# Optimization experiments

Measured on AMD Instinct MI355X. Metric: run time of the kernel, lower is better.

## Reference

```python
import jax, jax.numpy as jnp
import numpy as np
from jax import lax

H = 40            # hidden_size
IN = 257          # input_size / output bins
GRID_SIZE = 5     # efficient-kan defaults
SPLINE_ORDER = 3


def make_grid(in_features):
    # efficient-kan grid: arange(-k, G+k+1) * h + grid_range[0], grid_range=[-1,1]
    h = 2.0 / GRID_SIZE
    g = jnp.arange(-SPLINE_ORDER, GRID_SIZE + SPLINE_ORDER + 1, dtype=jnp.float32) * h - 1.0
    return jnp.broadcast_to(g, (in_features, g.shape[0]))  # (in, G+2k+1)


def b_splines(x, grid):
    # x: (N, in); grid: (in, G+2k+1) -> bases: (N, in, G+k) via Cox-de Boor
    xe = x[..., None]
    bases = ((xe >= grid[:, :-1]) & (xe < grid[:, 1:])).astype(x.dtype)
    for k in range(1, SPLINE_ORDER + 1):
        left = (xe - grid[:, :-(k + 1)]) / (grid[:, k:-1] - grid[:, :-(k + 1)])
        right = (grid[:, k + 1:] - xe) / (grid[:, k + 1:] - grid[:, 1:-k])
        bases = left * bases[..., :-1] + right * bases[..., 1:]
    return bases


def kan_linear(x, base_w, spline_w, scaler):
    # base_w: (out, in); spline_w: (out, in, G+k); scaler: (out, in)
    shp = x.shape
    x2 = x.reshape(-1, shp[-1])
    grid = make_grid(shp[-1])
    base = jax.nn.silu(x2) @ base_w.T
    sp = b_splines(x2, grid)                      # (N, in, G+k)
    scaled = spline_w * scaler[..., None]         # (out, in, G+k)
    spline = jnp.einsum('nig,oig->no', sp, scaled)
    out = base + spline
    return out.reshape(*shp[:-1], base_w.shape[0])


def gru_cell(x, h, Wih, Whh, bih, bhh):
    # torch GRUCell: gates ordered r, z, n
    gi = x @ Wih.T + bih
    gh = h @ Whh.T + bhh
    ir, iz, in_ = jnp.split(gi, 3, axis=-1)
    hr, hz, hn = jnp.split(gh, 3, axis=-1)
    r = jax.nn.sigmoid(ir + hr)
    z = jax.nn.sigmoid(iz + hz)
    n = jnp.tanh(in_ + r * hn)
    return (1.0 - z) * n + z * h


def run_gru(x_tbf, p0, p1):
    # x_tbf: (T, B, F); 2-layer stacked GRU scan, returns top-layer states (T, B, H)
    B = x_tbf.shape[1]
    def step(carry, xt):
        h0, h1 = carry
        h0 = gru_cell(xt, h0, *p0)
        h1 = gru_cell(h0, h1, *p1)
        return (h0, h1), h1
    init = (jnp.zeros((B, H), x_tbf.dtype), jnp.zeros((B, H), x_tbf.dtype))
    _, hs = lax.scan(step, init, x_tbf)
    return hs


def setup_inputs() -> dict:
    key = jax.random.key(0)
    ks = jax.random.split(key, 32)
    B, T = 64, 600
    s = 1.0 / np.sqrt(H)
    u = lambda k, shp: jax.random.uniform(k, shp, jnp.float32, -s, s)
    inp = {}
    inp['x'] = jax.random.normal(ks[0], (B, T, IN), jnp.float32)
    inp['lengths'] = jax.random.randint(ks[1], (B,), 1, T + 1, jnp.int32)
    i = 2
    for pre, insz in [('f0', IN), ('f1', H), ('b0', IN), ('b1', H)]:
        inp[pre + '_Wih'] = u(ks[i], (3 * H, insz)); i += 1
        inp[pre + '_Whh'] = u(ks[i], (3 * H, H)); i += 1
        inp[pre + '_bih'] = u(ks[i], (3 * H,)); i += 1
        inp[pre + '_bhh'] = u(ks[i], (3 * H,)); i += 1
    G = GRID_SIZE + SPLINE_ORDER
    inp['kan1_base'] = jax.random.normal(ks[i], (2 * H, 2 * H)) * 0.1; i += 1
    inp['kan1_spline'] = jax.random.normal(ks[i], (2 * H, 2 * H, G)) * 0.1; i += 1
    inp['kan1_scaler'] = jnp.ones((2 * H, 2 * H), jnp.float32)
    inp['kan2_base'] = jax.random.normal(ks[i], (IN, 2 * H)) * 0.1; i += 1
    inp['kan2_spline'] = jax.random.normal(ks[i], (IN, 2 * H, G)) * 0.1; i += 1
    inp['kan2_scaler'] = jnp.ones((IN, 2 * H), jnp.float32)
    inp['slope'] = jnp.ones((IN,), jnp.float32)
    return inp


def reference(x, lengths,
              f0_Wih, f0_Whh, f0_bih, f0_bhh,
              f1_Wih, f1_Whh, f1_bih, f1_bhh,
              b0_Wih, b0_Whh, b0_bih, b0_bhh,
              b1_Wih, b1_Whh, b1_bih, b1_bhh,
              kan1_base, kan1_spline, kan1_scaler,
              kan2_base, kan2_spline, kan2_scaler,
              slope):
    # lengths is unused by the original forward (kept for signature parity)
    xt = jnp.transpose(x, (1, 0, 2))  # (T, B, IN)
    hf = run_gru(xt, (f0_Wih, f0_Whh, f0_bih, f0_bhh), (f1_Wih, f1_Whh, f1_bih, f1_bhh))
    hb = run_gru(xt[::-1], (b0_Wih, b0_Whh, b0_bih, b0_bhh), (b1_Wih, b1_Whh, b1_bih, b1_bhh))
    # original stores concat(ht_f(i), ht_b(i)) at out[:, i]; ht_b(i) is step i of the
    # reversed-input scan, so NO flip of hb here.
    out = jnp.concatenate([hf, hb], axis=-1)        # (T, B, 2H)
    out = jnp.transpose(out, (1, 0, 2))             # (B, T, 2H)
    out = kan_linear(out, kan1_base, kan1_spline, kan1_scaler)
    out = kan_linear(out, kan2_base, kan2_spline, kan2_scaler)
    return 1.2 * jax.nn.sigmoid(slope * out)
```

## Files before the change

### kernel.cpp

```cpp
#include <hip/hip_runtime.h>
#include <cstdint>
#include <cstddef>

typedef unsigned short u16;
typedef unsigned int u32;
typedef __attribute__((ext_vector_type(8))) short short8;
typedef __attribute__((ext_vector_type(4))) float floatx4;
typedef __attribute__((ext_vector_type(2))) float float2v;

#define NROWS 38400

#define OFF_FLAG 0u
#define OFF_GI   64u
#define OFF_HCAT 36864064u
#define OFF_B1A  49152064u
#define OFF_B1B  49446976u
#define OFF_B2   49741888u
#define OFF_B3   49977408u

template<int N> struct IC { static constexpr int v = N; };

__device__ inline float bf2f(u16 u){ union{u32 i; float f;} v; v.i = ((u32)u)<<16; return v.f; }
__device__ inline u16 f2bf(float f){
  u32 u = __float_as_uint(f);
  return (u16)((u + 0x7FFFu + ((u>>16)&1u)) >> 16);
}
__device__ inline float lodf(const void* p, size_t i, int isbf){
  return isbf ? bf2f(((const u16*)p)[i]) : ((const float*)p)[i];
}
__device__ inline float rcpf(float x){ return __builtin_amdgcn_rcpf(x); }
__device__ inline float sigm(float x){ return rcpf(1.0f+__expf(-x)); }
__device__ inline float tanh_(float x){
  float e = __expf(-2.0f*fabsf(x)); float t = (1.0f-e)*rcpf(1.0f+e); return x<0.f ? -t : t;
}

__global__ void detect_kernel(const u16* __restrict__ xx, int* __restrict__ flag){
  const int l = threadIdx.x;
  const u16 w = xx[2*l];
  const int e = (w>>7)&0xFF;
  const unsigned long long m = __ballot(e >= 100 && e <= 133);
  if (l == 0) *flag = (__popcll(m) >= 32) ? 1 : 0;
}

__global__ void prep_kernel(const void* __restrict__ f0Wih, const void* __restrict__ b0Wih,
                            const void* __restrict__ k1b, const void* __restrict__ k1s, const void* __restrict__ k1sc,
                            const void* __restrict__ k2b, const void* __restrict__ k2s, const void* __restrict__ k2sc,
                            const int* __restrict__ flag,
                            u16* __restrict__ B1a, u16* __restrict__ B1b,
                            u16* __restrict__ B2, u16* __restrict__ B3)
{
  const int isbf = *flag;
  const int idx = blockIdx.x*256 + threadIdx.x;
  if (idx < 73728){
    const int j = idx/288, k = idx - j*288;
    float w = 0.f;
    if (k < 257 && j < 240)
      w = (j < 120) ? lodf(f0Wih, (size_t)j*257+k, isbf) : lodf(b0Wih, (size_t)(j-120)*257+k, isbf);
    const u16 hi = f2bf(w); const u16 lo = f2bf(w - bf2f(hi));
    B1a[(size_t)j*576 + 2*k] = hi; B1a[(size_t)j*576 + 2*k+1] = hi;
    B1b[(size_t)j*576 + 2*k] = lo; B1b[(size_t)j*576 + 2*k+1] = 0;
  } else if (idx < 132608){
    const int t = idx - 73728; const int n = t/736, m = t - n*736;
    float v = 0.f;
    if (m < 80) v = lodf(k1b, (size_t)n*80+m, isbf);
    else if (m >= 96){ const int m2 = m-96, i = m2>>3, g = m2&7;
      v = lodf(k1s, ((size_t)n*80+i)*8+g, isbf) * lodf(k1sc, (size_t)n*80+i, isbf); }
    const u16 vv = f2bf(v);
    B2[(size_t)n*1472 + 2*m] = vv; B2[(size_t)n*1472 + 2*m+1] = vv;
  } else {
    const int t = idx - 132608; const int n = t/736, m = t - n*736;
    float v = 0.f;
    if (n < 257){
      if (m < 80) v = lodf(k2b, (size_t)n*80+m, isbf);
      else if (m >= 96){ const int m2 = m-96, i = m2>>3, g = m2&7;
        v = lodf(k2s, ((size_t)n*80+i)*8+g, isbf) * lodf(k2sc, (size_t)n*80+i, isbf); }
    }
    const u16 vv = f2bf(v);
    B3[(size_t)n*1472 + 2*m] = vv; B3[(size_t)n*1472 + 2*m+1] = vv;
  }
}

__launch_bounds__(256)
__global__ void g1_kernel(const void* __restrict__ x, const u16* __restrict__ B1a, const u16* __restrict__ B1b,
                          const void* __restrict__ f0bih, const void* __restrict__ b0bih,
                          const int* __restrict__ flag, float* __restrict__ gi)
{
  __shared__ __attribute__((aligned(16))) u16 As[32][584];
  const int isbf = *flag;
  const int tid = threadIdx.x;
  const size_t r0 = (size_t)blockIdx.x * 32;
  const int w = tid>>6, l = tid&63, m16 = l&15, q4 = l>>4;
  const int cnt = (w<3)?4:3;
  const int ntlo = w*4;

  short8 bz;
  #pragma unroll
  for (int q=0;q<8;++q) bz[q]=0;
  short8 baC[4], bbC[4], baN[4], bbN[4];
  #pragma unroll
  for (int j=0;j<4;++j){ baC[j]=bz; bbC[j]=bz; baN[j]=bz; bbN[j]=bz; }
  #pragma unroll
  for (int j=0;j<4;++j) if (j<cnt){
    baC[j] = *(const short8*)&B1a[(size_t)((ntlo+j)*16+m16)*576 + q4*8];
    if (!isbf) bbC[j] = *(const short8*)&B1b[(size_t)((ntlo+j)*16+m16)*576 + q4*8];
  }

  {
    const int row = tid>>3, kk = tid&7;
    #pragma unroll
    for (int it=0; it<36; ++it){
      const int k = kk + it*8;
      const float v = (k < 257) ? lodf(x, (r0+row)*257 + k, isbf) : 0.f;
      const u16 hi = f2bf(v);
      As[row][2*k] = hi; As[row][2*k+1] = f2bf(v - bf2f(hi));
    }
  }
  __syncthreads();

  floatx4 acc[4][2];
  #pragma unroll
  for (int j=0;j<4;++j) for (int s=0;s<2;++s){ floatx4 z={0.f,0.f,0.f,0.f}; acc[j][s]=z; }
  #pragma unroll 1
  for (int ks=0; ks<18; ++ks){
    if (ks < 17){
      #pragma unroll
      for (int j=0;j<4;++j) if (j<cnt){
        baN[j] = *(const short8*)&B1a[(size_t)((ntlo+j)*16+m16)*576 + (ks+1)*32 + q4*8];
        if (!isbf) bbN[j] = *(const short8*)&B1b[(size_t)((ntlo+j)*16+m16)*576 + (ks+1)*32 + q4*8];
      }
    }
    const short8 a0 = *(const short8*)&As[m16][ks*32 + q4*8];
    const short8 a1 = *(const short8*)&As[16+m16][ks*32 + q4*8];
    #pragma unroll
    for (int j=0;j<4;++j){
      if (j < cnt){
        acc[j][0] = __builtin_amdgcn_mfma_f32_16x16x32_bf16(a0, baC[j], acc[j][0], 0, 0, 0);
        acc[j][1] = __builtin_amdgcn_mfma_f32_16x16x32_bf16(a1, baC[j], acc[j][1], 0, 0, 0);
        if (!isbf){
          acc[j][0] = __builtin_amdgcn_mfma_f32_16x16x32_bf16(a0, bbC[j], acc[j][0], 0, 0, 0);
          acc[j][1] = __builtin_amdgcn_mfma_f32_16x16x32_bf16(a1, bbC[j], acc[j][1], 0, 0, 0);
        }
      }
    }
    #pragma unroll
    for (int j=0;j<4;++j){ baC[j]=baN[j]; bbC[j]=bbN[j]; }
  }
  #pragma unroll
  for (int j=0;j<4;++j){
    if (j < cnt){
      const int col = (ntlo+j)*16 + m16;
      if (col < 240){
        const int dsel = (col < 120) ? 0 : 1;
        const int jj = (col < 120) ? col : col-120;
        const float bias = (col < 120) ? lodf(f0bih, col, isbf) : lodf(b0bih, col-120, isbf);
        #pragma unroll
        for (int s=0;s<2;++s){
          #pragma unroll
          for (int rg=0; rg<4; ++rg){
            const size_t row = r0 + s*16 + q4*4 + rg;
            gi[((size_t)dsel*NROWS + row)*120 + jj] = acc[j][s][rg] + bias;
          }
        }
      }
    }
  }
}

#define PIN_W() do { \
    _Pragma("unroll") \
    for (int k_ = 0; k_ < 20; ++k_) \
      asm volatile("" : "+v"(WA[k_]), "+v"(WB[k_]), "+v"(WC[k_])); \
    asm volatile("" : "+v"(bA), "+v"(bB), "+v"(bC)); \
  } while (0)

__device__ inline void stage_chunk32(const char* __restrict__ gid, int4* dst, int c, int d, int bat, int l)
{
  const long long rbase = (long long)bat*600 + (d ? (568 - 32*c) : (32*c));
  const long long base = rbase * 480;
  const long long lim = (long long)NROWS * 480;
  int4 v[15];
  #pragma unroll
  for (int j=0; j<15; ++j){
    const long long off = base + (long long)(j*64 + l)*16;
    int4 z; z.x=0; z.y=0; z.z=0; z.w=0;
    v[j] = (off >= 0 && off+16 <= lim) ? *(const int4*)(gid + off) : z;
  }
  #pragma unroll
  for (int j=0; j<15; ++j) dst[j*64 + l] = v[j];
}

__launch_bounds__(256, 1)
__global__ void gru_kernel(const float* __restrict__ gi,
  const void* __restrict__ f0Whh, const void* __restrict__ f0bhh,
  const void* __restrict__ f1Wih, const void* __restrict__ f1Whh, const void* __restrict__ f1bih, const void* __restrict__ f1bhh,
  const void* __restrict__ b0Whh, const void* __restrict__ b0bhh,
  const void* __restrict__ b1Wih, const void* __restrict__ b1Whh, const void* __restrict__ b1bih, const void* __restrict__ b1bhh,
  const int* __restrict__ flag, float* __restrict__ hcat)
{
  __shared__ int4 chunkbuf[2][960];
  __shared__ __attribute__((aligned(16))) float hbuf[2][64][40];
  __shared__ __attribute__((aligned(16))) float h0buf[2][4][40];
  __shared__ __attribute__((aligned(16))) float gi1buf[2][4][3][40];
  __shared__ __attribute__((aligned(16))) float h0st[40];
  __shared__ __attribute__((aligned(16))) float h1st[40];
  const int isbf = *flag;
  const int tid = threadIdx.x, l = tid&63;
  const int w = __builtin_amdgcn_readfirstlane(tid) >> 6;
  const int blk = blockIdx.x, d = blk>>6, bat = blk&63;
  const int li = (l < 40) ? l : 39;
  const char* gid = (const char*)(gi + (size_t)d*NROWS*120);

  if (w == 3){
    stage_chunk32(gid, &chunkbuf[0][0], 0, d, bat, l);
    __syncthreads();
    #pragma unroll 1
    for (int i=0; i<152; ++i){
      if ((i & 7) == 0){ const int c1 = (i>>3) + 1; if (c1 <= 18) stage_chunk32(gid, &chunkbuf[c1&1][0], c1, d, bat, l); }
      if ((i & 15) == 2 && i >= 18){
        const int m = (i>>4) - 1;
        const int t0 = 64*m;
        const int4* src = (const int4*)&hbuf[m&1][0][0];
        #pragma unroll
        for (int q=0; q<10; ++q){
          const int f = q*64 + l;
          const int t = f/10, j4 = f - 10*t;
          int4 v = src[t*10 + j4];
          *(int4*)&hcat[((size_t)bat*600 + t0 + t)*80 + d*40 + j4*4] = v;
        }
      }
      __syncthreads();
    }
  } else {
    const void *Wsrc = 0, *bsrc = 0;
    if (w == 0){ Wsrc = d ? b0Whh : f0Whh; bsrc = d ? b0bhh : f0bhh; }
    else if (w == 1){ Wsrc = d ? b1Wih : f1Wih; bsrc = d ? b1bih : f1bih; }
    else { Wsrc = d ? b1Whh : f1Whh; bsrc = d ? b1bhh : f1bhh; }

    float2v WA[20], WB[20], WC[20];
    #pragma unroll
    for (int k=0; k<20; ++k){
      WA[k][0] = lodf(Wsrc, (size_t)(     li)*40 + 2*k,   isbf);
      WA[k][1] = lodf(Wsrc, (size_t)(     li)*40 + 2*k+1, isbf);
      WB[k][0] = lodf(Wsrc, (size_t)(40 + li)*40 + 2*k,   isbf);
      WB[k][1] = lodf(Wsrc, (size_t)(40 + li)*40 + 2*k+1, isbf);
      WC[k][0] = lodf(Wsrc, (size_t)(80 + li)*40 + 2*k,   isbf);
      WC[k][1] = lodf(Wsrc, (size_t)(80 + li)*40 + 2*k+1, isbf);
    }
    float bA = lodf(bsrc, li, isbf), bB = lodf(bsrc, 40+li, isbf), bC = lodf(bsrc, 80+li, isbf);
    float hs = 0.f;

    auto mv3B = [&](const float* hrow, float& oa, float& ob, float& oc){
      float2v a2 = {bA, 0.f}, b2 = {bB, 0.f}, c2 = {bC, 0.f};
      #pragma unroll
      for (int kq=0; kq<10; ++kq){
        const floatx4 hv = *(const floatx4*)(hrow + kq*4);
        float2v h0; h0[0]=hv[0]; h0[1]=hv[1];
        float2v h1; h1[0]=hv[2]; h1[1]=hv[3];
        asm("v_pk_fma_f32 %0, %1, %2, %0" : "+v"(a2) : "v"(WA[2*kq  ]), "v"(h0));
        asm("v_pk_fma_f32 %0, %1, %2, %0" : "+v"(b2) : "v"(WB[2*kq  ]), "v"(h0));
        asm("v_pk_fma_f32 %0, %1, %2, %0" : "+v"(c2) : "v"(WC[2*kq  ]), "v"(h0));
        asm("v_pk_fma_f32 %0, %1, %2, %0" : "+v"(a2) : "v"(WA[2*kq+1]), "v"(h1));
        asm("v_pk_fma_f32 %0, %1, %2, %0" : "+v"(b2) : "v"(WB[2*kq+1]), "v"(h1));
        asm("v_pk_fma_f32 %0, %1, %2, %0" : "+v"(c2) : "v"(WC[2*kq+1]), "v"(h1));
      }
      oa = a2[0] + a2[1]; ob = b2[0] + b2[1]; oc = c2[0] + c2[1];
    };
    auto cellB = [&](const float* hrow, float hsv, float gA, float gB, float gC) -> float {
      float ar, az, an;
      mv3B(hrow, ar, az, an);
      const float r = sigm(gA + ar), z = sigm(gB + az);
      const float n = tanh_(gC + r*an);
      return (1.f - z)*n + z*hsv;
    };

    if (w == 0){
      if (l < 40) h0st[l] = 0.f;
      __syncthreads();
      #pragma unroll 1
      for (int i=0; i<152; ++i){
        PIN_W();
        if (i < 150){
          const int cc = (i>>3)&1;
          const int ta = (4*i)&31;
          const float* base = (const float*)&chunkbuf[cc][0];
          float gin[4][3];
          #pragma unroll
          for (int t=0; t<4; ++t){
            const float* r = base + (d ? (31-(ta+t)) : (ta+t))*120;
            gin[t][0]=r[li]; gin[t][1]=r[40+li]; gin[t][2]=r[80+li];
          }
          #pragma unroll
          for (int t=0; t<4; ++t){
            hs = cellB(h0st, hs, gin[t][0], gin[t][1], gin[t][2]);
            if (l < 40){ h0st[l] = hs; h0buf[i&1][t][l] = hs; }
          }
        }
        __syncthreads();
      }
    } else if (w == 1){
      __syncthreads();
      #pragma unroll 1
      for (int i=0; i<152; ++i){
        PIN_W();
        if (i >= 1 && i <= 150){
          const int p = (i-1)&1;
          #pragma unroll
          for (int t=0; t<4; ++t){
            float oa, ob, oc;
            mv3B(&h0buf[p][t][0], oa, ob, oc);
            if (l < 40){
              gi1buf[i&1][t][0][l]=oa; gi1buf[i&1][t][1][l]=ob; gi1buf[i&1][t][2][l]=oc;
            }
          }
        }
        __syncthreads();
      }
    } else {
      if (l < 40) h1st[l] = 0.f;
      __syncthreads();
      #pragma unroll 1
      for (int i=0; i<152; ++i){
        PIN_W();
        if (i >= 2){
          const int p = (i-1)&1;
          float gin[4][3];
          #pragma unroll
          for (int t=0; t<4; ++t){
            gin[t][0]=gi1buf[p][t][0][li]; gin[t][1]=gi1buf[p][t][1][li]; gin[t][2]=gi1buf[p][t][2][li];
          }
          const int ta2 = 4*(i-2);
          const int wp = (ta2>>6)&1, sa = ta2&63;
          #pragma unroll
          for (int t=0; t<4; ++t){
            hs = cellB(h1st, hs, gin[t][0], gin[t][1], gin[t][2]);
            if (l < 40){ h1st[l] = hs; hbuf[wp][sa+t][l] = hs; }
          }
        }
        __syncthreads();
      }
    }
  }
  if (tid < 240){
    const int t = tid/10, j4 = tid - 10*t;
    const int4* src = (const int4*)&hbuf[1][0][0];
    int4 v = src[t*10 + j4];
    *(int4*)&hcat[((size_t)bat*600 + 576 + t)*80 + d*40 + j4*4] = v;
  }
}

__launch_bounds__(256)
__global__ void kan_fused_kernel(const float* __restrict__ Xin,
                                 const u16* __restrict__ B2mat, const u16* __restrict__ B3mat,
                                 void* __restrict__ Obuf,
                                 const void* __restrict__ slope, const int* __restrict__ flag)
{
  __shared__ __attribute__((aligned(16))) float xs[64][84];
  __shared__ __attribute__((aligned(16))) u16 abase[64][200];
  __shared__ __attribute__((aligned(16))) u16 asp1[64][136];
  const int isbf = *flag;
  const int tid = threadIdx.x;
  const size_t r0 = (size_t)blockIdx.x * 64;
  const int w = tid>>6, l = tid&63, m16 = l&15, q4 = l>>4;

  for (int idx=tid; idx<5120; idx+=256){
    const int row = idx/80, m = idx - row*80;
    xs[row][m] = Xin[r0*80 + idx];
  }
  __syncthreads();

  auto spline_block = [&](int c, u16 (*dst)[136]){
    #pragma unroll
    for (int h=0; h<2; ++h){
      const int idx = tid + h*256;
      const int row = idx>>3, il = idx&7;
      const float xv = xs[row][c*8 + il];
      const float t  = (xv + 2.2f) * 2.5f;
      const float mf = fminf(fmaxf(floorf(t), -4.f), 14.f);
      const int   m  = (int)mf;
      const float u  = t - mf;
      const float u2 = u*u, u3 = u2*u;
      const float i6 = 1.0f/6.0f;
      const float w1mu = 1.f - u;
      const float n0 = w1mu*w1mu*w1mu*i6;
      const float n1 = (3.f*u3 - 6.f*u2 + 4.f)*i6;
      const float n2 = (-3.f*u3 + 3.f*u2 + 3.f*u + 1.f)*i6;
      const float n3 = u3*i6;
      const bool ok = (t >= 0.f) && (t < 11.f);
      union { u16 us[16]; short8 v2[2]; } pk;
      #pragma unroll
      for (int j=0; j<8; ++j){
        const int s = j + 3 - m;
        float v = 0.f;
        v = (s==0) ? n0 : v;
        v = (s==1) ? n1 : v;
        v = (s==2) ? n2 : v;
        v = (s==3) ? n3 : v;
        v = ok ? v : 0.f;
        const u16 hi = f2bf(v);
        pk.us[2*j] = hi; pk.us[2*j+1] = f2bf(v - bf2f(hi));
      }
      *(short8*)&dst[row][il*16]     = pk.v2[0];
      *(short8*)&dst[row][il*16 + 8] = pk.v2[1];
    }
  };

  auto phase = [&](auto ntc, auto fc, const u16* __restrict__ Bmat){
    constexpr int NT   = decltype(ntc)::v;
    constexpr int FINAL = decltype(fc)::v;
    constexpr int MAXC = (NT+3)/4;
    const int cbase = NT>>2, rem = NT&3;
    const int cnt  = cbase + ((w < rem) ? 1 : 0);
    const int ntlo = w*cbase + ((w < rem) ? w : rem);

    short8 bz;
    #pragma unroll
    for (int q=0;q<8;++q) bz[q]=0;
    short8 bcur[MAXC], bmid[MAXC], bnxt[MAXC];
    #pragma unroll
    for (int j=0;j<MAXC;++j){ bcur[j]=bz; bmid[j]=bz; bnxt[j]=bz; }

    #pragma unroll
    for (int j=0;j<MAXC;++j) if (j<cnt){
      bcur[j] = *(const short8*)&Bmat[(size_t)((ntlo+j)*16+m16)*1472 + 0*32 + q4*8];
      bmid[j] = *(const short8*)&Bmat[(size_t)((ntlo+j)*16+m16)*1472 + 1*32 + q4*8];
    }

    for (int idx=tid; idx<6144; idx+=256){
      const int row = idx/96, m = idx - row*96;
      float v = 0.f;
      if (m < 80){ const float xv = xs[row][m]; v = xv * sigm(xv); }
      const u16 hi = f2bf(v);
      abase[row][2*m] = hi; abase[row][2*m+1] = f2bf(v - bf2f(hi));
    }
    __syncthreads();

    floatx4 acc[MAXC][4];
    #pragma unroll
    for (int j=0;j<MAXC;++j) for (int s=0;s<4;++s){ floatx4 z={0.f,0.f,0.f,0.f}; acc[j][s]=z; }

    #pragma unroll 1
    for (int ks=0; ks<6; ++ks){
      if (ks < 4){
        #pragma unroll
        for (int j=0;j<MAXC;++j) if (j<cnt)
          bnxt[j] = *(const short8*)&Bmat[(size_t)((ntlo+j)*16+m16)*1472 + (ks+2)*32 + q4*8];
      }
      short8 a[4];
      #pragma unroll
      for (int s=0;s<4;++s) a[s] = *(const short8*)&abase[s*16+m16][ks*32 + q4*8];
      #pragma unroll
      for (int j=0;j<MAXC;++j){
        if (j < cnt){
          #pragma unroll
          for (int s=0;s<4;++s) acc[j][s] = __builtin_amdgcn_mfma_f32_16x16x32_bf16(a[s], bcur[j], acc[j][s], 0, 0, 0);
        }
      }
      #pragma unroll
      for (int j=0;j<MAXC;++j){ bcur[j]=bmid[j]; bmid[j]=bnxt[j]; }
    }
    __syncthreads();

    #pragma unroll
    for (int j=0;j<MAXC;++j) if (j<cnt){
      bcur[j] = *(const short8*)&Bmat[(size_t)((ntlo+j)*16+m16)*1472 + 192 + 0*128 + 0*32 + q4*8];
      bmid[j] = *(const short8*)&Bmat[(size_t)((ntlo+j)*16+m16)*1472 + 192 + 0*128 + 1*32 + q4*8];
    }
    spline_block(0, (u16(*)[136])&abase[0][0]);
    __syncthreads();

    #pragma unroll 1
    for (int c=0; c<10; ++c){
      if (c < 9) spline_block(c+1, ((c+1)&1) ? asp1 : (u16(*)[136])&abase[0][0]);
      const u16 (*aspr)[136] = (c&1) ? (const u16(*)[136])asp1 : (const u16(*)[136])&abase[0][0];
      #pragma unroll 1
      for (int ks=0; ks<4; ++ks){
        const int pos = c*4 + ks + 2;
        if (pos < 40){
          const int pc = pos>>2, pk = pos&3;
          #pragma unroll
          for (int j=0;j<MAXC;++j) if (j<cnt)
            bnxt[j] = *(const short8*)&Bmat[(size_t)((ntlo+j)*16+m16)*1472 + 192 + pc*128 + pk*32 + q4*8];
        }
        short8 a[4];
        #pragma unroll
        for (int s=0;s<4;++s) a[s] = *(const short8*)&aspr[s*16+m16][ks*32 + q4*8];
        #pragma unroll
        for (int j=0;j<MAXC;++j){
          if (j < cnt){
            #pragma unroll
            for (int s=0;s<4;++s) acc[j][s] = __builtin_amdgcn_mfma_f32_16x16x32_bf16(a[s], bcur[j], acc[j][s], 0, 0, 0);
          }
        }
        #pragma unroll
        for (int j=0;j<MAXC;++j){ bcur[j]=bmid[j]; bmid[j]=bnxt[j]; }
      }
      __syncthreads();
    }

    #pragma unroll
    for (int j=0;j<MAXC;++j){
      if (j < cnt){
        const int col = (ntlo+j)*16 + m16;
        #pragma unroll
        for (int s=0;s<4;++s){
          #pragma unroll
          for (int rg=0; rg<4; ++rg){
            const int row = s*16 + q4*4 + rg;
            const float v = acc[j][s][rg];
            if constexpr (!FINAL){
              xs[row][col] = v;
            } else {
              if (col < 257){
                const float sl = lodf(slope, col, isbf);
                const float o = 1.2f * sigm(sl*v);
                if (isbf) ((u16*)Obuf)[(r0+row)*257 + col] = f2bf(o);
                else      ((float*)Obuf)[(r0+row)*257 + col] = o;
              }
            }
          }
        }
      }
    }
    __syncthreads();
  };

  phase(IC<5>{},  IC<0>{}, B2mat);
  phase(IC<17>{}, IC<1>{}, B3mat);
}

extern "C" void kernel_launch(void* const* d_in, const int* in_sizes, int n_in,
                              void* d_out, int out_size, void* d_ws, size_t ws_size,
                              hipStream_t stream)
{
  (void)in_sizes; (void)n_in; (void)out_size; (void)ws_size;
  const void* x     = d_in[0];
  const void* f0Wih = d_in[2];  const void* f0Whh = d_in[3];
  const void* f0bih = d_in[4];  const void* f0bhh = d_in[5];
  const void* f1Wih = d_in[6];  const void* f1Whh = d_in[7];
  const void* f1bih = d_in[8];  const void* f1bhh = d_in[9];
  const void* b0Wih = d_in[10]; const void* b0Whh = d_in[11];
  const void* b0bih = d_in[12]; const void* b0bhh = d_in[13];
  const void* b1Wih = d_in[14]; const void* b1Whh = d_in[15];
  const void* b1bih = d_in[16]; const void* b1bhh = d_in[17];
  const void* k1b   = d_in[18]; const void* k1s   = d_in[19]; const void* k1sc = d_in[20];
  const void* k2b   = d_in[21]; const void* k2s   = d_in[22]; const void* k2sc = d_in[23];
  const void* slope = d_in[24];

  char* ws = (char*)d_ws;
  int*   flag  = (int*)(ws + OFF_FLAG);
  float* gi    = (float*)(ws + OFF_GI);
  float* hcat  = (float*)(ws + OFF_HCAT);
  u16* B1a = (u16*)(ws + OFF_B1A);
  u16* B1b = (u16*)(ws + OFF_B1B);
  u16* B2  = (u16*)(ws + OFF_B2);
  u16* B3  = (u16*)(ws + OFF_B3);

  detect_kernel<<<1, 64, 0, stream>>>((const u16*)x, flag);
  prep_kernel<<<1300, 256, 0, stream>>>(f0Wih, b0Wih, k1b, k1s, k1sc, k2b, k2s, k2sc, flag, B1a, B1b, B2, B3);
  g1_kernel<<<1200, 256, 0, stream>>>(x, B1a, B1b, f0bih, b0bih, flag, gi);
  gru_kernel<<<128, 256, 0, stream>>>(gi,
      f0Whh, f0bhh, f1Wih, f1Whh, f1bih, f1bhh,
      b0Whh, b0bhh, b1Wih, b1Whh, b1bih, b1bhh, flag, hcat);
  kan_fused_kernel<<<600, 256, 0, stream>>>(hcat, B2, B3, d_out, slope, flag);
}
```

Measured before the change: 581.3 us.

## Fuse layer-0 input projection GEMM into GRU kernel's staging wavefront

Removes the separate g1 GEMM kernel and the large gi workspace round-trip. The GRU kernel's fourth wavefront now computes each 32-step chunk of x·Wih with MFMA on the fly, spreading the 18 k-steps across 8 recurrence iterations, and writes the result with bias into the LDS chunk buffer. B1 weights are re-laid out so each direction occupies 128 padded rows. This saves the gi write/read and a launch, but the GEMM now runs on only 128 wavefronts alongside the serial recurrence and may stall the sync-paced loop if the per-iteration slice is slower than the recurrence step.

After: 1.288 ms. 122% more time.

```diff
diff --git a/kernel.cpp b/kernel.cpp
--- a/kernel.cpp
+++ b/kernel.cpp
@@ -53,9 +53,10 @@
   const int idx = blockIdx.x*256 + threadIdx.x;
   if (idx < 73728){
     const int j = idx/288, k = idx - j*288;
+    const int d = j>>7, jj = j&127;
     float w = 0.f;
-    if (k < 257 && j < 240)
-      w = (j < 120) ? lodf(f0Wih, (size_t)j*257+k, isbf) : lodf(b0Wih, (size_t)(j-120)*257+k, isbf);
+    if (k < 257 && jj < 120)
+      w = d ? lodf(b0Wih, (size_t)jj*257+k, isbf) : lodf(f0Wih, (size_t)jj*257+k, isbf);
     const u16 hi = f2bf(w); const u16 lo = f2bf(w - bf2f(hi));
     B1a[(size_t)j*576 + 2*k] = hi; B1a[(size_t)j*576 + 2*k+1] = hi;
     B1b[(size_t)j*576 + 2*k] = lo; B1b[(size_t)j*576 + 2*k+1] = 0;
@@ -80,92 +81,6 @@
   }
 }
 
-__launch_bounds__(256)
-__global__ void g1_kernel(const void* __restrict__ x, const u16* __restrict__ B1a, const u16* __restrict__ B1b,
-                          const void* __restrict__ f0bih, const void* __restrict__ b0bih,
-                          const int* __restrict__ flag, float* __restrict__ gi)
-{
-  __shared__ __attribute__((aligned(16))) u16 As[32][584];
-  const int isbf = *flag;
-  const int tid = threadIdx.x;
-  const size_t r0 = (size_t)blockIdx.x * 32;
-  const int w = tid>>6, l = tid&63, m16 = l&15, q4 = l>>4;
-  const int cnt = (w<3)?4:3;
-  const int ntlo = w*4;
-
-  short8 bz;
-  #pragma unroll
-  for (int q=0;q<8;++q) bz[q]=0;
-  short8 baC[4], bbC[4], baN[4], bbN[4];
-  #pragma unroll
-  for (int j=0;j<4;++j){ baC[j]=bz; bbC[j]=bz; baN[j]=bz; bbN[j]=bz; }
-  #pragma unroll
-  for (int j=0;j<4;++j) if (j<cnt){
-    baC[j] = *(const short8*)&B1a[(size_t)((ntlo+j)*16+m16)*576 + q4*8];
-    if (!isbf) bbC[j] = *(const short8*)&B1b[(size_t)((ntlo+j)*16+m16)*576 + q4*8];
-  }
-
-  {
-    const int row = tid>>3, kk = tid&7;
-    #pragma unroll
-    for (int it=0; it<36; ++it){
-      const int k = kk + it*8;
-      const float v = (k < 257) ? lodf(x, (r0+row)*257 + k, isbf) : 0.f;
-      const u16 hi = f2bf(v);
-      As[row][2*k] = hi; As[row][2*k+1] = f2bf(v - bf2f(hi));
-    }
-  }
-  __syncthreads();
-
-  floatx4 acc[4][2];
-  #pragma unroll
-  for (int j=0;j<4;++j) for (int s=0;s<2;++s){ floatx4 z={0.f,0.f,0.f,0.f}; acc[j][s]=z; }
-  #pragma unroll 1
-  for (int ks=0; ks<18; ++ks){
-    if (ks < 17){
-      #pragma unroll
-      for (int j=0;j<4;++j) if (j<cnt){
-        baN[j] = *(const short8*)&B1a[(size_t)((ntlo+j)*16+m16)*576 + (ks+1)*32 + q4*8];
-        if (!isbf) bbN[j] = *(const short8*)&B1b[(size_t)((ntlo+j)*16+m16)*576 + (ks+1)*32 + q4*8];
-      }
-    }
-    const short8 a0 = *(const short8*)&As[m16][ks*32 + q4*8];
-    const short8 a1 = *(const short8*)&As[16+m16][ks*32 + q4*8];
-    #pragma unroll
-    for (int j=0;j<4;++j){
-      if (j < cnt){
-        acc[j][0] = __builtin_amdgcn_mfma_f32_16x16x32_bf16(a0, baC[j], acc[j][0], 0, 0, 0);
-        acc[j][1] = __builtin_amdgcn_mfma_f32_16x16x32_bf16(a1, baC[j], acc[j][1], 0, 0, 0);
-        if (!isbf){
-          acc[j][0] = __builtin_amdgcn_mfma_f32_16x16x32_bf16(a0, bbC[j], acc[j][0], 0, 0, 0);
-          acc[j][1] = __builtin_amdgcn_mfma_f32_16x16x32_bf16(a1, bbC[j], acc[j][1], 0, 0, 0);
-        }
-      }
-    }
-    #pragma unroll
-    for (int j=0;j<4;++j){ baC[j]=baN[j]; bbC[j]=bbN[j]; }
-  }
-  #pragma unroll
-  for (int j=0;j<4;++j){
-    if (j < cnt){
-      const int col = (ntlo+j)*16 + m16;
-      if (col < 240){
-        const int dsel = (col < 120) ? 0 : 1;
-        const int jj = (col < 120) ? col : col-120;
-        const float bias = (col < 120) ? lodf(f0bih, col, isbf) : lodf(b0bih, col-120, isbf);
-        #pragma unroll
-        for (int s=0;s<2;++s){
-          #pragma unroll
-          for (int rg=0; rg<4; ++rg){
-            const size_t row = r0 + s*16 + q4*4 + rg;
-            gi[((size_t)dsel*NROWS + row)*120 + jj] = acc[j][s][rg] + bias;
-          }
-        }
-      }
-    }
-  }
-}
-
 #define PIN_W() do { \
     _Pragma("unroll") \
     for (int k_ = 0; k_ < 20; ++k_) \
@@ -173,24 +88,10 @@
     asm volatile("" : "+v"(bA), "+v"(bB), "+v"(bC)); \
   } while (0)
 
-__device__ inline void stage_chunk32(const char* __restrict__ gid, int4* dst, int c, int d, int bat, int l)
-{
-  const long long rbase = (long long)bat*600 + (d ? (568 - 32*c) : (32*c));
-  const long long base = rbase * 480;
-  const long long lim = (long long)NROWS * 480;
-  int4 v[15];
-  #pragma unroll
-  for (int j=0; j<15; ++j){
-    const long long off = base + (long long)(j*64 + l)*16;
-    int4 z; z.x=0; z.y=0; z.z=0; z.w=0;
-    v[j] = (off >= 0 && off+16 <= lim) ? *(const int4*)(gid + off) : z;
-  }
-  #pragma unroll
-  for (int j=0; j<15; ++j) dst[j*64 + l] = v[j];
-}
-
 __launch_bounds__(256, 1)
-__global__ void gru_kernel(const float* __restrict__ gi,
+__global__ void gru_kernel(const void* __restrict__ x,
+  const u16* __restrict__ B1a, const u16* __restrict__ B1b,
+  const void* __restrict__ f0bih, const void* __restrict__ b0bih,
   const void* __restrict__ f0Whh, const void* __restrict__ f0bhh,
   const void* __restrict__ f1Wih, const void* __restrict__ f1Whh, const void* __restrict__ f1bih, const void* __restrict__ f1bhh,
   const void* __restrict__ b0Whh, const void* __restrict__ b0bhh,
@@ -208,14 +109,92 @@
   const int w = __builtin_amdgcn_readfirstlane(tid) >> 6;
   const int blk = blockIdx.x, d = blk>>6, bat = blk&63;
   const int li = (l < 40) ? l : 39;
-  const char* gid = (const char*)(gi + (size_t)d*NROWS*120);
+  const int m16 = l&15, q4 = l>>4;
 
   if (w == 3){
-    stage_chunk32(gid, &chunkbuf[0][0], 0, d, bat, l);
+    const u16* B1ad = B1a + (size_t)(d ? 128 : 0)*576;
+    const u16* B1bd = B1b + (size_t)(d ? 128 : 0)*576;
+    const void* bihd = d ? b0bih : f0bih;
+    float bias_v[8];
+    #pragma unroll
+    for (int nt=0; nt<8; ++nt){
+      const int col = nt*16 + m16;
+      bias_v[nt] = (col < 120) ? lodf(bihd, col, isbf) : 0.f;
+    }
+    const long long xrow0 = (long long)bat*600;
+
+    floatx4 acc[2][8];
+
+    auto acc_zero = [&](){
+      #pragma unroll
+      for (int mt=0;mt<2;++mt)
+        #pragma unroll
+        for (int nt=0;nt<8;++nt){ floatx4 z={0.f,0.f,0.f,0.f}; acc[mt][nt]=z; }
+    };
+    auto afrag = [&](int tick0, int mt, int ks) -> short8 {
+      int t = tick0 + mt*16 + m16;
+      t = (t < 0) ? 0 : (t > 599 ? 599 : t);
+      const size_t xb = (size_t)(xrow0 + t)*257;
+      short8 af;
+      #pragma unroll
+      for (int cj=0; cj<4; ++cj){
+        const int col = ks*16 + q4*4 + cj;
+        const float v = (col < 257) ? lodf(x, xb + col, isbf) : 0.f;
+        const u16 hi = f2bf(v);
+        af[2*cj]   = (short)hi;
+        af[2*cj+1] = (short)f2bf(v - bf2f(hi));
+      }
+      return af;
+    };
+    auto chunk_ks = [&](int c, int k0, int k1){
+      const int tick0 = d ? (568 - 32*c) : (32*c);
+      #pragma unroll 1
+      for (int ks=k0; ks<k1; ++ks){
+        const short8 af0 = afrag(tick0, 0, ks);
+        const short8 af1 = afrag(tick0, 1, ks);
+        #pragma unroll
+        for (int nt=0; nt<8; ++nt){
+          const short8 ba = *(const short8*)&B1ad[(size_t)(nt*16+m16)*576 + ks*32 + q4*8];
+          acc[0][nt] = __builtin_amdgcn_mfma_f32_16x16x32_bf16(af0, ba, acc[0][nt], 0, 0, 0);
+          acc[1][nt] = __builtin_amdgcn_mfma_f32_16x16x32_bf16(af1, ba, acc[1][nt], 0, 0, 0);
+          if (!isbf){
+            const short8 bb = *(const short8*)&B1bd[(size_t)(nt*16+m16)*576 + ks*32 + q4*8];
+            acc[0][nt] = __builtin_amdgcn_mfma_f32_16x16x32_bf16(af0, bb, acc[0][nt], 0, 0, 0);
+            acc[1][nt] = __builtin_amdgcn_mfma_f32_16x16x32_bf16(af1, bb, acc[1][nt], 0, 0, 0);
+          }
+        }
+      }
+    };
+    auto chunk_store = [&](int c){
+      float* dst = (float*)&chunkbuf[c&1][0];
+      #pragma unroll
+      for (int mt=0; mt<2; ++mt){
+        #pragma unroll
+        for (int nt=0; nt<8; ++nt){
+          const int col = nt*16 + m16;
+          if (col < 120){
+            #pragma unroll
+            for (int rg=0; rg<4; ++rg){
+              const int tick = mt*16 + q4*4 + rg;
+              dst[tick*120 + col] = acc[mt][nt][rg] + bias_v[nt];
+            }
+          }
+        }
+      }
+    };
+
+    acc_zero();
+    chunk_ks(0, 0, 18);
+    chunk_store(0);
     __syncthreads();
     #pragma unroll 1
     for (int i=0; i<152; ++i){
-      if ((i & 7) == 0){ const int c1 = (i>>3) + 1; if (c1 <= 18) stage_chunk32(gid, &chunkbuf[c1&1][0], c1, d, bat, l); }
+      const int c1 = (i>>3) + 1, s = i&7;
+      if (c1 <= 18){
+        if (s == 0) acc_zero();
+        chunk_ks(c1, (s*18)>>3, ((s+1)*18)>>3);
+        if (s == 7) chunk_store(c1);
+      }
       if ((i & 15) == 2 && i >= 18){
         const int m = (i>>4) - 1;
         const int t0 = 64*m;
@@ -548,7 +527,6 @@
 
   char* ws = (char*)d_ws;
   int*   flag  = (int*)(ws + OFF_FLAG);
-  float* gi    = (float*)(ws + OFF_GI);
   float* hcat  = (float*)(ws + OFF_HCAT);
   u16* B1a = (u16*)(ws + OFF_B1A);
   u16* B1b = (u16*)(ws + OFF_B1B);
@@ -557,8 +535,7 @@
 
   detect_kernel<<<1, 64, 0, stream>>>((const u16*)x, flag);
   prep_kernel<<<1300, 256, 0, stream>>>(f0Wih, b0Wih, k1b, k1s, k1sc, k2b, k2s, k2sc, flag, B1a, B1b, B2, B3);
-  g1_kernel<<<1200, 256, 0, stream>>>(x, B1a, B1b, f0bih, b0bih, flag, gi);
-  gru_kernel<<<128, 256, 0, stream>>>(gi,
+  gru_kernel<<<128, 256, 0, stream>>>(x, B1a, B1b, f0bih, b0bih,
       f0Whh, f0bhh, f1Wih, f1Whh, f1bih, f1bhh,
       b0Whh, b0bhh, b1Wih, b1Whh, b1bih, b1bhh, flag, hcat);
   kan_fused_kernel<<<600, 256, 0, stream>>>(hcat, B2, B3, d_out, slope, flag);
```
